# Kernel optimization log

Hardware: AMD Instinct MI355X
Metric: run time of the kernel (lower is better)

The kernel has to match this reference:

```python
import jax, jax.numpy as jnp
import numpy as np

B, N, F_IN, F_OUT, H = 8, 1024, 128, 64, 4
EPS = 1e-7
NEG_SLOPE = 0.2


def setup_inputs() -> dict:
    key = jax.random.key(0)
    k_a, k_x, k_w, k_aw, k_ab = jax.random.split(key, 5)
    A = jax.random.randint(k_a, (B, N, N), 0, 2).astype(jnp.float32)
    x = jax.random.normal(k_x, (B, N, F_IN), dtype=jnp.float32)
    # per-head params (stacked over head axis): GAT.W (xavier-normal-ish), attention Linear(2F->1)
    W = jax.random.normal(k_w, (H, F_IN, F_OUT), dtype=jnp.float32) * np.sqrt(2.0 / (F_IN + F_OUT))
    lim = 1.0 / np.sqrt(2 * F_OUT)
    a_w = jax.random.uniform(k_aw, (H, 2 * F_OUT), minval=-lim, maxval=lim, dtype=jnp.float32)
    a_b = jax.random.uniform(k_ab, (H,), minval=-lim, maxval=lim, dtype=jnp.float32)
    return {"A": A, "x": x, "W": W, "a_w": a_w, "a_b": a_b}


def reference(A, x, W, a_w, a_b):
    # Wh: (B, H, N, F_OUT)
    Wh = jnp.einsum('bnf,hfo->bhno', x, W)
    # attention linear on concat([Wh_i, Wh_j]) is separable: a1.Wh_i + a2.Wh_j + b
    a1, a2 = a_w[:, :F_OUT], a_w[:, F_OUT:]
    s_i = jnp.einsum('bhno,ho->bhn', Wh, a1)   # depends on row index i (dim 1 of (B,N,N))
    s_j = jnp.einsum('bhno,ho->bhn', Wh, a2)   # depends on col index j (dim 2)
    e = s_i[:, :, :, None] + s_j[:, :, None, :] + a_b[None, :, None, None]  # (B,H,Ni,Nj)
    e = jnp.where(e >= 0, e, NEG_SLOPE * e)  # LeakyReLU(0.2)
    # masked softmax as in source: exp, mask by A, normalize over dim=1 of (B,N,N) -> axis 2 here
    exps = jnp.exp(e) * A[:, None, :, :]
    attn = exps / (jnp.sum(exps, axis=2, keepdims=True) + EPS)
    out = jnp.einsum('bhij,bhjo->bhio', attn, Wh)  # matmul over j
    # concat heads on feature dim: (B, N, H*F_OUT)
    return out.transpose(0, 2, 1, 3).reshape(B, N, H * F_OUT)
```

## Files before the change

### kernel.cpp

```cpp
#include <hip/hip_runtime.h>
#include <hip/hip_bf16.h>
#include <hip/hip_fp16.h>

#define BB 8
#define NN 1024
#define FIN 128
#define FOUT 64
#define HH 4
#define EPSV 1e-7f
#define SLOPE 0.2f
#define LOG2E 1.44269504088896340736f

typedef _Float16 v8h __attribute__((ext_vector_type(8)));
typedef _Float16 v4h __attribute__((ext_vector_type(4)));
typedef __fp16 v2hf __attribute__((ext_vector_type(2)));
typedef float v4f __attribute__((ext_vector_type(4)));

__global__ __launch_bounds__(256) void k0_wt(const float* __restrict__ W,
                                             _Float16* __restrict__ Wtt) {
  for (int it = 0; it < 16; ++it) {
    int idx = blockIdx.x * 4096 + it * 256 + threadIdx.x;
    int e = idx & 7, ln = (idx >> 3) & 15, kgg = (idx >> 7) & 15,
        ct = idx >> 11;
    int c = ct * 16 + ln, k = kgg * 8 + e;
    Wtt[idx] = (_Float16)W[(size_t)(c >> 6) * 8192 + k * 64 + (c & 63)];
  }
}

__global__ __launch_bounds__(256) void k1_whm(const float* __restrict__ x,
                                              const _Float16* __restrict__ Wtt,
                                              const float* __restrict__ aw,
                                              const float* __restrict__ ab,
                                              _Float16* __restrict__ WhH,
                                              float* __restrict__ si2,
                                              float* __restrict__ tj2) {
  __shared__ _Float16 xs[16][136];
  int tid = threadIdx.x;
#pragma unroll
  for (int t2 = 0; t2 < 2; ++t2) {
    int idx = t2 * 256 + tid;
    int row = idx >> 5, c4 = (idx & 31) * 4;
    float4 v = *(const float4*)(x + ((size_t)blockIdx.x * 16 + row) * FIN + c4);
    v4h hv;
    hv[0] = (_Float16)v.x; hv[1] = (_Float16)v.y;
    hv[2] = (_Float16)v.z; hv[3] = (_Float16)v.w;
    *(v4h*)(&xs[row][c4]) = hv;
  }
  __syncthreads();
  int w = tid >> 6, l = tid & 63;
  int kg = l >> 4, ln = l & 15;
  v4f acc[4] = {{}, {}, {}, {}};
#pragma unroll
  for (int ks = 0; ks < 4; ++ks) {
    v8h af = *(const v8h*)(&xs[ln][ks * 32 + kg * 8]);
    int kgg = ks * 4 + kg;
#pragma unroll
    for (int t = 0; t < 4; ++t) {
      int ct = w * 4 + t;
      v8h bf = *(const v8h*)(Wtt + (((size_t)ct * 16 + kgg) * 16 + ln) * 8);
      acc[t] = __builtin_amdgcn_mfma_f32_16x16x32_f16(af, bf, acc[t], 0, 0, 0);
    }
  }
  float a1v[4], a2v[4];
#pragma unroll
  for (int t = 0; t < 4; ++t) {
    a1v[t] = aw[w * 128 + t * 16 + ln];
    a2v[t] = aw[w * 128 + 64 + t * 16 + ln];
  }
  float abv = ab[w];
#pragma unroll
  for (int r = 0; r < 4; ++r) {
    float v1 = acc[0][r] * a1v[0] + acc[1][r] * a1v[1] +
               acc[2][r] * a1v[2] + acc[3][r] * a1v[3];
    float v2 = acc[0][r] * a2v[0] + acc[1][r] * a2v[1] +
               acc[2][r] * a2v[2] + acc[3][r] * a2v[3];
#pragma unroll
    for (int off = 1; off < 16; off <<= 1) {
      v1 += __shfl_xor(v1, off);
      v2 += __shfl_xor(v2, off);
    }
    if (ln == 0) {
      int gr = blockIdx.x * 16 + kg * 4 + r;
      int b_ = gr >> 10, n_ = gr & 1023;
      size_t row = ((size_t)b_ * HH + w) * NN + n_;
      si2[row] = v1 * LOG2E;
      tj2[row] = (v2 + abv) * LOG2E;
    }
  }
#pragma unroll
  for (int t = 0; t < 4; ++t) {
#pragma unroll
    for (int r = 0; r < 4; ++r) {
      int gr = blockIdx.x * 16 + kg * 4 + r;
      int b_ = gr >> 10, n_ = gr & 1023;
      WhH[(((size_t)b_ * HH + w) * NN + n_) * 64 + (t * 16 + ln)] =
          (_Float16)acc[t][r];
    }
  }
}

__global__ __launch_bounds__(256) void kb_colsum_bits(
    const float* __restrict__ A, const float* __restrict__ si2,
    const float* __restrict__ tj2, float* __restrict__ part,
    unsigned long long* __restrict__ Abits) {
  __shared__ float sil[4][32];
  int b = blockIdx.z, is = blockIdx.y, jt = blockIdx.x;
  int tid = threadIdx.x;
  int w = tid >> 6, lane = tid & 63;
  int j = jt * 256 + tid;
  int i0 = is * 32;
  if (tid < 128) {
    int h = tid >> 5, ii = tid & 31;
    sil[h][ii] = si2[((size_t)(b * HH + h)) * NN + i0 + ii];
  }
  __syncthreads();
  float tjv[4], acc[4] = {0.f, 0.f, 0.f, 0.f};
#pragma unroll
  for (int h = 0; h < 4; ++h) tjv[h] = tj2[((size_t)(b * HH + h)) * NN + j];
  const float* Ap = A + ((size_t)b * NN + i0) * NN + j;
  unsigned long long myword = 0ull;
#pragma unroll
  for (int c = 0; c < 4; ++c) {
    float av[8];
#pragma unroll
    for (int q = 0; q < 8; ++q)
      av[q] = Ap[(size_t)(c * 8 + q) * NN];
#pragma unroll
    for (int q = 0; q < 8; ++q) {
      unsigned long long m = __ballot(av[q] != 0.0f);
      if (lane == c * 8 + q) myword = m;
      int ii = c * 8 + q;
#pragma unroll
      for (int h = 0; h < 4; ++h) {
        float f = sil[h][ii] + tjv[h];
        float g = fmaxf(f, SLOPE * f);
        acc[h] += av[q] * __builtin_amdgcn_exp2f(g);
      }
    }
  }
  if (lane < 32)
    Abits[((size_t)b * NN + i0 + lane) * 16 + jt * 4 + w] = myword;
#pragma unroll
  for (int h = 0; h < 4; ++h)
    part[((size_t)(is * 32) + b * HH + h) * NN + j] = acc[h];
}

__global__ __launch_bounds__(256) void k3_scale_tr(
    const _Float16* __restrict__ WhH, const float* __restrict__ part,
    _Float16* __restrict__ VTt) {
  __shared__ float rbuf[64];
  __shared__ _Float16 tile[64 * 66];
  int bid = blockIdx.x;
  int b = bid & 7, rest = bid >> 3;
  int h = rest & 3, jt = rest >> 2;
  int bh = b * HH + h, j0 = jt * 64;
  int tid = threadIdx.x;
  if (tid < 64) {
    float s = 0.f;
#pragma unroll
    for (int is = 0; is < 32; ++is)
      s += part[((size_t)(is * 32) + bh) * NN + j0 + tid];
    rbuf[tid] = 1.0f / (s + EPSV);
  }
  __syncthreads();
#pragma unroll
  for (int it = 0; it < 16; ++it) {
    int lin = it * 256 + tid;
    int jj = lin >> 6, o = lin & 63;
    float v = (float)WhH[((size_t)bh * NN + j0 + jj) * 64 + o] * rbuf[jj];
    tile[o * 66 + jj] = (_Float16)v;
  }
  __syncthreads();
#pragma unroll
  for (int it = 0; it < 16; ++it) {
    int lin = it * 256 + tid;
    int o = lin >> 6, jj64 = lin & 63;
    int j = j0 + jj64;
    int jb = j >> 5, jj = j & 31;
    VTt[(((size_t)bh * 32 + jb) * 64 + o) * 32 + jj] = tile[o * 66 + jj64];
  }
}

__global__ __launch_bounds__(512, 4) void k4_pv(
    const unsigned long long* __restrict__ Abits,
    const float* __restrict__ si2, const float* __restrict__ tj2,
    const _Float16* __restrict__ VTt, float* __restrict__ out) {
  __shared__ unsigned long long Ab[32][17];
  __shared__ float tjl[2][1024];
  __shared__ float sil[2][32];
  __shared__ float red[2][2][64][32];
  int bid = blockIdx.x;
  int b = bid & 7, hp = (bid >> 3) & 1, it = bid >> 4;
  int i0 = it * 32;
  int tid = threadIdx.x;
#pragma unroll
  for (int t2 = 0; t2 < 4; ++t2) {
    int idx = t2 * 512 + tid;
    int hh = idx >> 10, j = idx & 1023;
    tjl[hh][j] = tj2[((size_t)(b * HH + hp * 2 + hh)) * NN + j];
  }
  if (tid < 64) {
    int hh = tid >> 5, ii = tid & 31;
    sil[hh][ii] = si2[((size_t)(b * HH + hp * 2 + hh)) * NN + i0 + ii];
  }
  {
    int row = tid >> 4, word = tid & 15;
    if (word < 16) Ab[row][word] = Abits[((size_t)b * NN + i0 + row) * 16 + word];
  }
  __syncthreads();

  int w = tid >> 6, l = tid & 63;
  int hh = w & 1, jq4 = w >> 1;
  int kg = l >> 4, ln = l & 15;
  float si0 = sil[hh][ln];
  float si1 = sil[hh][16 + ln];
  int bh = b * HH + hp * 2 + hh;
  v4f acc0[4] = {{}, {}, {}, {}};
  v4f acc1[4] = {{}, {}, {}, {}};
  const _Float16* VTb = VTt + (size_t)bh * 32 * 64 * 32;
  const float* tj = tjl[hh];
  int jbase = jq4 * 256;

#define PEXP(si, tv) \
  __builtin_amdgcn_exp2f(fmaxf((si) + (tv), SLOPE * ((si) + (tv))))

#pragma unroll 2
  for (int jq = 0; jq < 8; ++jq) {
    int j = jbase + jq * 32 + kg * 8;
    int widx = j >> 6, sh = j & 63;
    unsigned int bits0 = (unsigned int)(Ab[ln][widx] >> sh) & 0xffu;
    unsigned int bits1 = (unsigned int)(Ab[16 + ln][widx] >> sh) & 0xffu;
    float4 t0 = *(const float4*)(tj + j);
    float4 t1 = *(const float4*)(tj + j + 4);
    float p0[8], p1[8];
    p0[0] = (bits0 & 1u) ? PEXP(si0, t0.x) : 0.f;
    p0[1] = (bits0 & 2u) ? PEXP(si0, t0.y) : 0.f;
    p0[2] = (bits0 & 4u) ? PEXP(si0, t0.z) : 0.f;
    p0[3] = (bits0 & 8u) ? PEXP(si0, t0.w) : 0.f;
    p0[4] = (bits0 & 16u) ? PEXP(si0, t1.x) : 0.f;
    p0[5] = (bits0 & 32u) ? PEXP(si0, t1.y) : 0.f;
    p0[6] = (bits0 & 64u) ? PEXP(si0, t1.z) : 0.f;
    p0[7] = (bits0 & 128u) ? PEXP(si0, t1.w) : 0.f;
    p1[0] = (bits1 & 1u) ? PEXP(si1, t0.x) : 0.f;
    p1[1] = (bits1 & 2u) ? PEXP(si1, t0.y) : 0.f;
    p1[2] = (bits1 & 4u) ? PEXP(si1, t0.z) : 0.f;
    p1[3] = (bits1 & 8u) ? PEXP(si1, t0.w) : 0.f;
    p1[4] = (bits1 & 16u) ? PEXP(si1, t1.x) : 0.f;
    p1[5] = (bits1 & 32u) ? PEXP(si1, t1.y) : 0.f;
    p1[6] = (bits1 & 64u) ? PEXP(si1, t1.z) : 0.f;
    p1[7] = (bits1 & 128u) ? PEXP(si1, t1.w) : 0.f;
    union { v2hf h2[4]; v8h h8; } u0, u1;
#pragma unroll
    for (int q = 0; q < 4; ++q) {
      u0.h2[q] = __builtin_amdgcn_cvt_pkrtz(p0[2 * q], p0[2 * q + 1]);
      u1.h2[q] = __builtin_amdgcn_cvt_pkrtz(p1[2 * q], p1[2 * q + 1]);
    }
    v8h af0 = u0.h8, af1 = u1.h8;
    const _Float16* vb = VTb + (size_t)(j >> 5) * 2048 + kg * 8;
    v8h b0 = *(const v8h*)(vb + (0 * 16 + ln) * 32);
    v8h b1 = *(const v8h*)(vb + (1 * 16 + ln) * 32);
    v8h b2 = *(const v8h*)(vb + (2 * 16 + ln) * 32);
    v8h b3 = *(const v8h*)(vb + (3 * 16 + ln) * 32);
    acc0[0] = __builtin_amdgcn_mfma_f32_16x16x32_f16(af0, b0, acc0[0], 0, 0, 0);
    acc1[0] = __builtin_amdgcn_mfma_f32_16x16x32_f16(af1, b0, acc1[0], 0, 0, 0);
    acc0[1] = __builtin_amdgcn_mfma_f32_16x16x32_f16(af0, b1, acc0[1], 0, 0, 0);
    acc1[1] = __builtin_amdgcn_mfma_f32_16x16x32_f16(af1, b1, acc1[1], 0, 0, 0);
    acc0[2] = __builtin_amdgcn_mfma_f32_16x16x32_f16(af0, b2, acc0[2], 0, 0, 0);
    acc1[2] = __builtin_amdgcn_mfma_f32_16x16x32_f16(af1, b2, acc1[2], 0, 0, 0);
    acc0[3] = __builtin_amdgcn_mfma_f32_16x16x32_f16(af0, b3, acc0[3], 0, 0, 0);
    acc1[3] = __builtin_amdgcn_mfma_f32_16x16x32_f16(af1, b3, acc1[3], 0, 0, 0);
  }
#undef PEXP

  if (jq4 == 1 || jq4 == 3) {
    int slot = jq4 >> 1;
#pragma unroll
    for (int t = 0; t < 4; ++t)
#pragma unroll
      for (int r = 0; r < 4; ++r) {
        red[hh][slot][l][t * 4 + r] = acc0[t][r];
        red[hh][slot][l][16 + t * 4 + r] = acc1[t][r];
      }
  }
  __syncthreads();
  if (jq4 == 0 || jq4 == 2) {
    int slot = jq4 >> 1;
#pragma unroll
    for (int t = 0; t < 4; ++t)
#pragma unroll
      for (int r = 0; r < 4; ++r) {
        acc0[t][r] += red[hh][slot][l][t * 4 + r];
        acc1[t][r] += red[hh][slot][l][16 + t * 4 + r];
      }
  }
  __syncthreads();
  if (jq4 == 2) {
#pragma unroll
    for (int t = 0; t < 4; ++t)
#pragma unroll
      for (int r = 0; r < 4; ++r) {
        red[hh][0][l][t * 4 + r] = acc0[t][r];
        red[hh][0][l][16 + t * 4 + r] = acc1[t][r];
      }
  }
  __syncthreads();
  if (jq4 == 0) {
#pragma unroll
    for (int t = 0; t < 4; ++t)
#pragma unroll
      for (int r = 0; r < 4; ++r) {
        acc0[t][r] += red[hh][0][l][t * 4 + r];
        acc1[t][r] += red[hh][0][l][16 + t * 4 + r];
      }
#pragma unroll
    for (int r = 0; r < 4; ++r) {
      int gi0 = i0 + kg * 4 + r;
      float* op0 = out + ((size_t)b * NN + gi0) * 256 + (hp * 2 + hh) * 64;
      op0[0 * 16 + ln] = acc0[0][r];
      op0[1 * 16 + ln] = acc0[1][r];
      op0[2 * 16 + ln] = acc0[2][r];
      op0[3 * 16 + ln] = acc0[3][r];
      float* op1 = op0 + 16 * 256;
      op1[0 * 16 + ln] = acc1[0][r];
      op1[1 * 16 + ln] = acc1[1][r];
      op1[2 * 16 + ln] = acc1[2][r];
      op1[3 * 16 + ln] = acc1[3][r];
    }
  }
}

extern "C" void kernel_launch(void* const* d_in, const int* in_sizes, int n_in,
                              void* d_out, int out_size, void* d_ws,
                              size_t ws_size, hipStream_t stream) {
  const float* A = (const float*)d_in[0];
  const float* x = (const float*)d_in[1];
  const float* W = (const float*)d_in[2];
  const float* aw = (const float*)d_in[3];
  const float* ab = (const float*)d_in[4];
  float* out = (float*)d_out;
  char* ws = (char*)d_ws;
  _Float16* WhH = (_Float16*)ws;
  _Float16* VTt = (_Float16*)(ws + (4u << 20));
  _Float16* Wtt = (_Float16*)(ws + (8u << 20));
  float* si2 = (float*)(ws + (8u << 20) + (256u << 10));
  float* tj2 = (float*)(ws + (8u << 20) + (384u << 10));
  float* part = (float*)(ws + (8u << 20) + (512u << 10));
  unsigned long long* Abits =
      (unsigned long long*)(ws + (12u << 20) + (512u << 10));

  hipLaunchKernelGGL(k0_wt, dim3(8), dim3(256), 0, stream, W, Wtt);
  hipLaunchKernelGGL(k1_whm, dim3(512), dim3(256), 0, stream, x, Wtt, aw, ab,
                     WhH, si2, tj2);
  hipLaunchKernelGGL(kb_colsum_bits, dim3(4, 32, BB), dim3(256), 0, stream, A,
                     si2, tj2, part, Abits);
  hipLaunchKernelGGL(k3_scale_tr, dim3(512), dim3(256), 0, stream, WhH, part,
                     VTt);
  hipLaunchKernelGGL(k4_pv, dim3(512), dim3(512), 0, stream, Abits, si2, tj2,
                     VTt, out);
}
```

Measured before the change: 48.60 us.

## Factor masked leaky-exp into precomputed per-row/col exponentials with packed fp16 math

The k4 attention kernel no longer evaluates exp2 per (i,j) element. It uses the identity exp(leaky(si+tj)) = exp(si)exp(tj) when si+tj≥0 and exp(0.2si)exp(0.2tj) otherwise. k1 now precomputes the per-row and per-column exponentials and their differences. k4 builds each weight from a saturated fp16 step selector and packed half2 FMAs, and applies the mask via a shared-memory bit-to-half lookup table. This replaces transcendental work and per-bit branches with packed fp16 arithmetic, but the sign test and products now run in fp16, which reduces precision and risks overflow of exp values.

Result: faster. 45.64 us (-6.1%).

```diff
diff --git a/kernel.cpp b/kernel.cpp
--- a/kernel.cpp
+++ b/kernel.cpp
@@ -13,8 +13,16 @@
 
 typedef _Float16 v8h __attribute__((ext_vector_type(8)));
 typedef _Float16 v4h __attribute__((ext_vector_type(4)));
-typedef __fp16 v2hf __attribute__((ext_vector_type(2)));
+typedef _Float16 v2h __attribute__((ext_vector_type(2)));
 typedef float v4f __attribute__((ext_vector_type(4)));
+
+union U8 { v2h p[4]; v8h v; };
+
+__device__ __forceinline__ v2h clamp01(v2h x) {
+  v2h zero = {(_Float16)0.0f, (_Float16)0.0f};
+  v2h one = {(_Float16)1.0f, (_Float16)1.0f};
+  return __builtin_elementwise_min(__builtin_elementwise_max(x, zero), one);
+}
 
 __global__ __launch_bounds__(256) void k0_wt(const float* __restrict__ W,
                                              _Float16* __restrict__ Wtt) {
@@ -27,13 +35,13 @@
   }
 }
 
-__global__ __launch_bounds__(256) void k1_whm(const float* __restrict__ x,
-                                              const _Float16* __restrict__ Wtt,
-                                              const float* __restrict__ aw,
-                                              const float* __restrict__ ab,
-                                              _Float16* __restrict__ WhH,
-                                              float* __restrict__ si2,
-                                              float* __restrict__ tj2) {
+__global__ __launch_bounds__(256) void k1_whm(
+    const float* __restrict__ x, const _Float16* __restrict__ Wtt,
+    const float* __restrict__ aw, const float* __restrict__ ab,
+    _Float16* __restrict__ WhH, float* __restrict__ si2,
+    float* __restrict__ tj2, _Float16* __restrict__ tjh,
+    _Float16* __restrict__ djh, _Float16* __restrict__ e2jh,
+    float* __restrict__ e2i_t, float* __restrict__ di_t) {
   __shared__ _Float16 xs[16][136];
   int tid = threadIdx.x;
 #pragma unroll
@@ -83,8 +91,19 @@
       int gr = blockIdx.x * 16 + kg * 4 + r;
       int b_ = gr >> 10, n_ = gr & 1023;
       size_t row = ((size_t)b_ * HH + w) * NN + n_;
-      si2[row] = v1 * LOG2E;
-      tj2[row] = (v2 + abv) * LOG2E;
+      float v1L = v1 * LOG2E;
+      float tjL = (v2 + abv) * LOG2E;
+      si2[row] = v1L;
+      tj2[row] = tjL;
+      float e1i = __builtin_amdgcn_exp2f(v1L);
+      float e2i = __builtin_amdgcn_exp2f(0.2f * v1L);
+      e2i_t[row] = e2i;
+      di_t[row] = e1i - e2i;
+      float e1j = __builtin_amdgcn_exp2f(tjL);
+      float e2j = __builtin_amdgcn_exp2f(0.2f * tjL);
+      tjh[row] = (_Float16)tjL;
+      e2jh[row] = (_Float16)e2j;
+      djh[row] = (_Float16)(e1j - e2j);
     }
   }
 #pragma unroll
@@ -123,8 +142,7 @@
   for (int c = 0; c < 4; ++c) {
     float av[8];
 #pragma unroll
-    for (int q = 0; q < 8; ++q)
-      av[q] = Ap[(size_t)(c * 8 + q) * NN];
+    for (int q = 0; q < 8; ++q) av[q] = Ap[(size_t)(c * 8 + q) * NN];
 #pragma unroll
     for (int q = 0; q < 8; ++q) {
       unsigned long long m = __ballot(av[q] != 0.0f);
@@ -183,46 +201,67 @@
 
 __global__ __launch_bounds__(512, 4) void k4_pv(
     const unsigned long long* __restrict__ Abits,
-    const float* __restrict__ si2, const float* __restrict__ tj2,
+    const float* __restrict__ si2, const _Float16* __restrict__ tjh,
+    const _Float16* __restrict__ djh, const _Float16* __restrict__ e2jh,
+    const float* __restrict__ e2i_t, const float* __restrict__ di_t,
     const _Float16* __restrict__ VTt, float* __restrict__ out) {
   __shared__ unsigned long long Ab[32][17];
-  __shared__ float tjl[2][1024];
-  __shared__ float sil[2][32];
-  __shared__ float red[2][2][64][32];
+  __shared__ _Float16 tjl[2][1024];
+  __shared__ _Float16 djl[2][1024];
+  __shared__ _Float16 e2jl[2][1024];
+  __shared__ _Float16 lut[256][8];
+  __shared__ float sil[2][32], e2il[2][32], dil[2][32];
+  __shared__ float red[2][2][64][33];
   int bid = blockIdx.x;
   int b = bid & 7, hp = (bid >> 3) & 1, it = bid >> 4;
   int i0 = it * 32;
   int tid = threadIdx.x;
-#pragma unroll
-  for (int t2 = 0; t2 < 4; ++t2) {
-    int idx = t2 * 512 + tid;
-    int hh = idx >> 10, j = idx & 1023;
-    tjl[hh][j] = tj2[((size_t)(b * HH + hp * 2 + hh)) * NN + j];
+  {
+    size_t base = (size_t)(b * HH + hp * 2) * NN;
+    const unsigned int* s1 = (const unsigned int*)(tjh + base);
+    const unsigned int* s2 = (const unsigned int*)(djh + base);
+    const unsigned int* s3 = (const unsigned int*)(e2jh + base);
+    unsigned int* d1 = (unsigned int*)&tjl[0][0];
+    unsigned int* d2 = (unsigned int*)&djl[0][0];
+    unsigned int* d3 = (unsigned int*)&e2jl[0][0];
+    d1[tid] = s1[tid]; d1[tid + 512] = s1[tid + 512];
+    d2[tid] = s2[tid]; d2[tid + 512] = s2[tid + 512];
+    d3[tid] = s3[tid]; d3[tid + 512] = s3[tid + 512];
   }
   if (tid < 64) {
     int hh = tid >> 5, ii = tid & 31;
-    sil[hh][ii] = si2[((size_t)(b * HH + hp * 2 + hh)) * NN + i0 + ii];
+    size_t row = (size_t)(b * HH + hp * 2 + hh) * NN + i0 + ii;
+    sil[hh][ii] = si2[row];
+    e2il[hh][ii] = e2i_t[row];
+    dil[hh][ii] = di_t[row];
+  }
+  if (tid < 256) {
+#pragma unroll
+    for (int e = 0; e < 8; ++e)
+      lut[tid][e] = ((tid >> e) & 1) ? (_Float16)1.0f : (_Float16)0.0f;
   }
   {
     int row = tid >> 4, word = tid & 15;
-    if (word < 16) Ab[row][word] = Abits[((size_t)b * NN + i0 + row) * 16 + word];
+    Ab[row][word] = Abits[((size_t)b * NN + i0 + row) * 16 + word];
   }
   __syncthreads();
 
   int w = tid >> 6, l = tid & 63;
   int hh = w & 1, jq4 = w >> 1;
   int kg = l >> 4, ln = l & 15;
-  float si0 = sil[hh][ln];
-  float si1 = sil[hh][16 + ln];
+  _Float16 sih0 = (_Float16)sil[hh][ln];
+  _Float16 sih1 = (_Float16)sil[hh][16 + ln];
+  v2h si0 = {sih0, sih0}, si1 = {sih1, sih1};
+  _Float16 e2h0 = (_Float16)e2il[hh][ln], e2h1 = (_Float16)e2il[hh][16 + ln];
+  _Float16 dih0 = (_Float16)dil[hh][ln], dih1 = (_Float16)dil[hh][16 + ln];
+  v2h e2i0 = {e2h0, e2h0}, e2i1 = {e2h1, e2h1};
+  v2h di0 = {dih0, dih0}, di1 = {dih1, dih1};
+  v2h big = {(_Float16)4096.0f, (_Float16)4096.0f};
   int bh = b * HH + hp * 2 + hh;
   v4f acc0[4] = {{}, {}, {}, {}};
   v4f acc1[4] = {{}, {}, {}, {}};
   const _Float16* VTb = VTt + (size_t)bh * 32 * 64 * 32;
-  const float* tj = tjl[hh];
   int jbase = jq4 * 256;
-
-#define PEXP(si, tv) \
-  __builtin_amdgcn_exp2f(fmaxf((si) + (tv), SLOPE * ((si) + (tv))))
 
 #pragma unroll 2
   for (int jq = 0; jq < 8; ++jq) {
@@ -230,47 +269,39 @@
     int widx = j >> 6, sh = j & 63;
     unsigned int bits0 = (unsigned int)(Ab[ln][widx] >> sh) & 0xffu;
     unsigned int bits1 = (unsigned int)(Ab[16 + ln][widx] >> sh) & 0xffu;
-    float4 t0 = *(const float4*)(tj + j);
-    float4 t1 = *(const float4*)(tj + j + 4);
-    float p0[8], p1[8];
-    p0[0] = (bits0 & 1u) ? PEXP(si0, t0.x) : 0.f;
-    p0[1] = (bits0 & 2u) ? PEXP(si0, t0.y) : 0.f;
-    p0[2] = (bits0 & 4u) ? PEXP(si0, t0.z) : 0.f;
-    p0[3] = (bits0 & 8u) ? PEXP(si0, t0.w) : 0.f;
-    p0[4] = (bits0 & 16u) ? PEXP(si0, t1.x) : 0.f;
-    p0[5] = (bits0 & 32u) ? PEXP(si0, t1.y) : 0.f;
-    p0[6] = (bits0 & 64u) ? PEXP(si0, t1.z) : 0.f;
-    p0[7] = (bits0 & 128u) ? PEXP(si0, t1.w) : 0.f;
-    p1[0] = (bits1 & 1u) ? PEXP(si1, t0.x) : 0.f;
-    p1[1] = (bits1 & 2u) ? PEXP(si1, t0.y) : 0.f;
-    p1[2] = (bits1 & 4u) ? PEXP(si1, t0.z) : 0.f;
-    p1[3] = (bits1 & 8u) ? PEXP(si1, t0.w) : 0.f;
-    p1[4] = (bits1 & 16u) ? PEXP(si1, t1.x) : 0.f;
-    p1[5] = (bits1 & 32u) ? PEXP(si1, t1.y) : 0.f;
-    p1[6] = (bits1 & 64u) ? PEXP(si1, t1.z) : 0.f;
-    p1[7] = (bits1 & 128u) ? PEXP(si1, t1.w) : 0.f;
-    union { v2hf h2[4]; v8h h8; } u0, u1;
+    U8 tj8, dj8, ej8, m0, m1, af0, af1;
+    tj8.v = *(const v8h*)&tjl[hh][j];
+    dj8.v = *(const v8h*)&djl[hh][j];
+    ej8.v = *(const v8h*)&e2jl[hh][j];
+    m0.v = *(const v8h*)&lut[bits0][0];
+    m1.v = *(const v8h*)&lut[bits1][0];
 #pragma unroll
     for (int q = 0; q < 4; ++q) {
-      u0.h2[q] = __builtin_amdgcn_cvt_pkrtz(p0[2 * q], p0[2 * q + 1]);
-      u1.h2[q] = __builtin_amdgcn_cvt_pkrtz(p1[2 * q], p1[2 * q + 1]);
-    }
-    v8h af0 = u0.h8, af1 = u1.h8;
+      v2h f0 = tj8.p[q] + si0;
+      v2h s0 = clamp01(f0 * big);
+      v2h ej0 = s0 * dj8.p[q] + ej8.p[q];
+      v2h ei0 = s0 * di0 + e2i0;
+      af0.p[q] = ei0 * ej0 * m0.p[q];
+      v2h f1 = tj8.p[q] + si1;
+      v2h s1v = clamp01(f1 * big);
+      v2h ej1 = s1v * dj8.p[q] + ej8.p[q];
+      v2h ei1 = s1v * di1 + e2i1;
+      af1.p[q] = ei1 * ej1 * m1.p[q];
+    }
     const _Float16* vb = VTb + (size_t)(j >> 5) * 2048 + kg * 8;
     v8h b0 = *(const v8h*)(vb + (0 * 16 + ln) * 32);
     v8h b1 = *(const v8h*)(vb + (1 * 16 + ln) * 32);
     v8h b2 = *(const v8h*)(vb + (2 * 16 + ln) * 32);
     v8h b3 = *(const v8h*)(vb + (3 * 16 + ln) * 32);
-    acc0[0] = __builtin_amdgcn_mfma_f32_16x16x32_f16(af0, b0, acc0[0], 0, 0, 0);
-    acc1[0] = __builtin_amdgcn_mfma_f32_16x16x32_f16(af1, b0, acc1[0], 0, 0, 0);
-    acc0[1] = __builtin_amdgcn_mfma_f32_16x16x32_f16(af0, b1, acc0[1], 0, 0, 0);
-    acc1[1] = __builtin_amdgcn_mfma_f32_16x16x32_f16(af1, b1, acc1[1], 0, 0, 0);
-    acc0[2] = __builtin_amdgcn_mfma_f32_16x16x32_f16(af0, b2, acc0[2], 0, 0, 0);
-    acc1[2] = __builtin_amdgcn_mfma_f32_16x16x32_f16(af1, b2, acc1[2], 0, 0, 0);
-    acc0[3] = __builtin_amdgcn_mfma_f32_16x16x32_f16(af0, b3, acc0[3], 0, 0, 0);
-    acc1[3] = __builtin_amdgcn_mfma_f32_16x16x32_f16(af1, b3, acc1[3], 0, 0, 0);
-  }
-#undef PEXP
+    acc0[0] = __builtin_amdgcn_mfma_f32_16x16x32_f16(af0.v, b0, acc0[0], 0, 0, 0);
+    acc1[0] = __builtin_amdgcn_mfma_f32_16x16x32_f16(af1.v, b0, acc1[0], 0, 0, 0);
+    acc0[1] = __builtin_amdgcn_mfma_f32_16x16x32_f16(af0.v, b1, acc0[1], 0, 0, 0);
+    acc1[1] = __builtin_amdgcn_mfma_f32_16x16x32_f16(af1.v, b1, acc1[1], 0, 0, 0);
+    acc0[2] = __builtin_amdgcn_mfma_f32_16x16x32_f16(af0.v, b2, acc0[2], 0, 0, 0);
+    acc1[2] = __builtin_amdgcn_mfma_f32_16x16x32_f16(af1.v, b2, acc1[2], 0, 0, 0);
+    acc0[3] = __builtin_amdgcn_mfma_f32_16x16x32_f16(af0.v, b3, acc0[3], 0, 0, 0);
+    acc1[3] = __builtin_amdgcn_mfma_f32_16x16x32_f16(af1.v, b3, acc1[3], 0, 0, 0);
+  }
 
   if (jq4 == 1 || jq4 == 3) {
     int slot = jq4 >> 1;
@@ -347,14 +378,20 @@
   float* part = (float*)(ws + (8u << 20) + (512u << 10));
   unsigned long long* Abits =
       (unsigned long long*)(ws + (12u << 20) + (512u << 10));
+  char* tb = ws + (13u << 20) + (512u << 10);
+  _Float16* tjh = (_Float16*)tb;
+  _Float16* djh = (_Float16*)(tb + (64u << 10));
+  _Float16* e2jh = (_Float16*)(tb + (128u << 10));
+  float* e2i_t = (float*)(tb + (192u << 10));
+  float* di_t = (float*)(tb + (320u << 10));
 
   hipLaunchKernelGGL(k0_wt, dim3(8), dim3(256), 0, stream, W, Wtt);
   hipLaunchKernelGGL(k1_whm, dim3(512), dim3(256), 0, stream, x, Wtt, aw, ab,
-                     WhH, si2, tj2);
+                     WhH, si2, tj2, tjh, djh, e2jh, e2i_t, di_t);
   hipLaunchKernelGGL(kb_colsum_bits, dim3(4, 32, BB), dim3(256), 0, stream, A,
                      si2, tj2, part, Abits);
   hipLaunchKernelGGL(k3_scale_tr, dim3(512), dim3(256), 0, stream, WhH, part,
                      VTt);
-  hipLaunchKernelGGL(k4_pv, dim3(512), dim3(512), 0, stream, Abits, si2, tj2,
-                     VTt, out);
-}
+  hipLaunchKernelGGL(k4_pv, dim3(512), dim3(512), 0, stream, Abits, si2, tjh,
+                     djh, e2jh, e2i_t, di_t, VTt, out);
+}
```
